# Kernel optimization log

Hardware: AMD Instinct MI355X
Metric: run time of the kernel (lower is better)

Reference implementation:

```python
import jax, jax.numpy as jnp
import numpy as np

B, T = 8, 1024
D = 256          # n_embd
NH = 4           # n_head
MULT = 4         # mlp_internal_dim_multiplier
GRID = 32        # grid_size, T == GRID*GRID
NLAYER = 3
N = D * MULT // NH   # sparse head dim = 256
EPS = 1e-5


def _freqs_2d(h, w, dim, theta=10000.0):
    # matches get_freqs_2d_fixed: returns (h*w, dim//2) complex64
    dim_half = dim // 2
    freqs = 1.0 / theta ** (np.arange(0, dim_half, 2, dtype=np.float32) / dim_half)
    fx = np.outer(np.arange(w, dtype=np.float32), freqs)
    fy = np.outer(np.arange(h, dtype=np.float32), freqs)
    cx = np.exp(1j * fx).astype(np.complex64)          # (w, dim_half/2)
    cy = np.exp(1j * fy).astype(np.complex64)          # (h, dim_half/2)
    gx = np.broadcast_to(cx[None, :, :], (h, w, cx.shape[-1]))
    gy = np.broadcast_to(cy[:, None, :], (h, w, cy.shape[-1]))
    return np.concatenate([gx, gy], axis=-1).reshape(h * w, -1)

FREQS = jnp.asarray(_freqs_2d(GRID, GRID, N))  # (T, N//2) complex64


def _rope(x):
    # x: (B, nh, T, N) real -> complex pairs, rotate, back to real
    xc = x.reshape(*x.shape[:-1], -1, 2)
    xc = jax.lax.complex(xc[..., 0], xc[..., 1])       # (B, nh, T, N/2)
    xr = xc * FREQS[None, None, :, :]
    out = jnp.stack([jnp.real(xr), jnp.imag(xr)], axis=-1)
    return out.reshape(x.shape).astype(x.dtype)


def _ln(x):
    # LayerNorm over last dim, no affine (biased variance, like torch)
    m = jnp.mean(x, axis=-1, keepdims=True)
    v = jnp.var(x, axis=-1, keepdims=True)
    return (x - m) / jnp.sqrt(v + EPS)


def setup_inputs() -> dict:
    key = jax.random.key(0)
    ks = jax.random.split(key, 6)
    std = 0.02
    return {
        "inputs": jax.random.normal(ks[0], (B, T), dtype=jnp.float32),
        "in_w": jax.random.normal(ks[1], (D, 1), dtype=jnp.float32) * std,
        "in_b": jnp.zeros((D,), dtype=jnp.float32),
        "encoder": jax.random.normal(ks[2], (NH, D, N), dtype=jnp.float32) * std,
        "encoder_v": jax.random.normal(ks[3], (NH, D, N), dtype=jnp.float32) * std,
        "decoder": jax.random.normal(ks[4], (NH * N, D), dtype=jnp.float32) * std,
        "out_w": jax.random.normal(ks[5], (1, D), dtype=jnp.float32) * std,
        "out_b": jnp.zeros((1,), dtype=jnp.float32),
    }


def reference(inputs, in_w, in_b, encoder, encoder_v, decoder, out_w, out_b):
    # input projection: (B,T,1) @ (1,D) + b -> (B,T,D)
    x = inputs[..., None] * in_w[None, None, :, 0].swapaxes(-1, -1)  # placeholder
    x = inputs[..., None] @ in_w.T + in_b                            # (B,T,D)
    x = _ln(x)
    scale = 1.0 / jnp.sqrt(jnp.asarray(N, dtype=x.dtype))
    for _ in range(NLAYER):
        # encoder: (B,T,D) x (nh,D,N) -> (B,nh,T,N)
        x_sparse = jax.nn.relu(jnp.einsum('btd,hdn->bhtn', x, encoder))
        QR = _rope(x_sparse)
        KR = _rope(x_sparse)
        scores = jnp.einsum('bhtn,bhsn->bhts', QR, KR) * scale       # (B,nh,T,T)
        attn = jax.nn.softmax(scores, axis=-1)
        yKV = jnp.einsum('bhts,bsd->bhtd', attn, x)                  # V = x, broadcast over heads
        yKV = _ln(yKV)
        y_sparse = jax.nn.relu(jnp.einsum('bhtd,hdn->bhtn', yKV, encoder_v))
        xy_sparse = x_sparse * y_sparse                              # (B,nh,T,N)
        # (B,nh,T,N) -> (B,T,nh*N) @ (nh*N,D) -> (B,T,D)
        yMLP = xy_sparse.transpose(0, 2, 1, 3).reshape(B, T, NH * N) @ decoder
        x = _ln(x + _ln(yMLP))
    logits = x @ out_w.T + out_b                                     # (B,T,1)
    return logits
```

## Files before the change

### kernel.cpp

```cpp
#include <hip/hip_runtime.h>
#include <hip/hip_bf16.h>
#include <math.h>

#define B_ 8
#define T_ 1024
#define D_ 256
#define NH_ 4
#define N_ 256
#define EPS_ 1e-5f

typedef __attribute__((ext_vector_type(8))) short short8_t;
typedef __attribute__((ext_vector_type(4))) float floatx4;

__device__ inline unsigned short f2bf(float f) {
    unsigned u = __builtin_bit_cast(unsigned, f);
    u += 0x7FFFu + ((u >> 16) & 1u);
    return (unsigned short)(u >> 16);
}
__device__ inline float bf2f(unsigned short h) {
    return __builtin_bit_cast(float, (unsigned)h << 16);
}

__device__ inline void gload_lds16(const unsigned short* g, unsigned short* l) {
    __builtin_amdgcn_global_load_lds(
        (const __attribute__((address_space(1))) unsigned int*)g,
        (__attribute__((address_space(3))) unsigned int*)l, 16, 0, 0);
}

__device__ inline float2 block_stats_256(float v, float* red) {
    float s1 = v, s2 = v * v;
    #pragma unroll
    for (int o = 32; o > 0; o >>= 1) { s1 += __shfl_down(s1, o); s2 += __shfl_down(s2, o); }
    int wave = threadIdx.x >> 6, lane = threadIdx.x & 63;
    __syncthreads();
    if (lane == 0) { red[wave] = s1; red[4 + wave] = s2; }
    __syncthreads();
    float S1 = red[0] + red[1] + red[2] + red[3];
    float S2 = red[4] + red[5] + red[6] + red[7];
    float mean = S1 * (1.f / 256.f);
    float var  = S2 * (1.f / 256.f) - mean * mean;
    return make_float2(mean, var);
}

__global__ __launch_bounds__(256) void k_wT(
    const float* __restrict__ in, unsigned short* __restrict__ outh,
    unsigned short* __restrict__ outl, int R, int C)
{
    __shared__ float tile[64][65];
    int c0 = blockIdx.x * 64, r0 = blockIdx.y * 64, h = blockIdx.z;
    in += (size_t)h * R * C;
    for (int i = threadIdx.x; i < 4096; i += 256) {
        int r = i >> 6, c = i & 63;
        tile[r][c] = in[(size_t)(r0 + r) * C + c0 + c];
    }
    __syncthreads();
    for (int i = threadIdx.x; i < 4096; i += 256) {
        int c = i >> 6, r = i & 63;
        float v = tile[r][c];
        unsigned short hb = f2bf(v);
        size_t o = (size_t)(h * C + c0 + c) * R + r0 + r;
        outh[o] = hb;
        outl[o] = f2bf(v - bf2f(hb));
    }
}

__global__ __launch_bounds__(256) void k_input_ln(
    const float* __restrict__ inputs, const float* __restrict__ in_w,
    const float* __restrict__ in_b, float* __restrict__ x,
    unsigned short* __restrict__ xh, unsigned short* __restrict__ xl)
{
    __shared__ float red[8];
    int row = blockIdx.x;
    int d = threadIdx.x;
    float v = inputs[row] * in_w[d] + in_b[d];
    float2 mv = block_stats_256(v, red);
    float o = (v - mv.x) * rsqrtf(mv.y + EPS_);
    size_t idx = (size_t)row * D_ + d;
    x[idx] = o;
    unsigned short hb = f2bf(o);
    xh[idx] = hb;
    xl[idx] = f2bf(o - bf2f(hb));
}

#define PG 40
template<int MODE>
__global__ __launch_bounds__(256, 2) void k_gemm_mfma(
    const unsigned short* __restrict__ Ah, const unsigned short* __restrict__ Al,
    const unsigned short* __restrict__ Wh, const unsigned short* __restrict__ Wl,
    const unsigned short* __restrict__ xsh, const unsigned short* __restrict__ xsl,
    unsigned short* __restrict__ outh, unsigned short* __restrict__ outl,
    float* __restrict__ outf,
    unsigned short* __restrict__ qrh, unsigned short* __restrict__ qrl)
{
    constexpr int K = (MODE == 2) ? 1024 : 256;
    __shared__ unsigned short As_h[128 * PG], As_l[128 * PG];
    __shared__ unsigned short Ws_h[128 * PG], Ws_l[128 * PG];
    int tid = threadIdx.x;
    int w = tid >> 6, lane = tid & 63, quad = lane >> 4, l16 = lane & 15;
    int wm = w >> 1, wn = w & 1;
    int m0 = blockIdx.y * 128, n0x = blockIdx.x * 128;
    size_t a_row0, w_row0, out_row0;
    int col0;
    int koff = 0, kend = K;
    if (MODE == 1) {
        int bh = blockIdx.z;
        a_row0 = (size_t)bh * 1024 + m0;
        w_row0 = (size_t)((bh & 3) * 256 + n0x);
        out_row0 = (size_t)(bh >> 2) * 1024 + m0;
        col0 = (bh & 3) * 256 + n0x;
    } else {
        a_row0 = m0; w_row0 = n0x; out_row0 = m0; col0 = n0x;
        if (MODE == 2) { koff = blockIdx.z * 256; kend = koff + 256; }
    }
    floatx4 acc[4][4];
    #pragma unroll
    for (int mt = 0; mt < 4; mt++)
        #pragma unroll
        for (int nt = 0; nt < 4; nt++)
            acc[mt][nt] = (floatx4){0.f, 0.f, 0.f, 0.f};

    for (int k0 = koff; k0 < kend; k0 += 32) {
        #pragma unroll
        for (int it = 0; it < 2; it++) {
            int fl = tid + it * 256;
            int row = fl >> 2, ch = fl & 3;
            size_t ga = (a_row0 + row) * (size_t)K + k0 + ch * 8;
            size_t gw = (w_row0 + row) * (size_t)K + k0 + ch * 8;
            *(short8_t*)&As_h[row * PG + ch * 8] = *(const short8_t*)(Ah + ga);
            *(short8_t*)&As_l[row * PG + ch * 8] = *(const short8_t*)(Al + ga);
            *(short8_t*)&Ws_h[row * PG + ch * 8] = *(const short8_t*)(Wh + gw);
            *(short8_t*)&Ws_l[row * PG + ch * 8] = *(const short8_t*)(Wl + gw);
        }
        __syncthreads();
        short8_t afh[4], afl[4], bfh[4], bfl[4];
        #pragma unroll
        for (int mt = 0; mt < 4; mt++) {
            afh[mt] = *(const short8_t*)&As_h[(wm * 64 + mt * 16 + l16) * PG + quad * 8];
            afl[mt] = *(const short8_t*)&As_l[(wm * 64 + mt * 16 + l16) * PG + quad * 8];
        }
        #pragma unroll
        for (int nt = 0; nt < 4; nt++) {
            bfh[nt] = *(const short8_t*)&Ws_h[(wn * 64 + nt * 16 + l16) * PG + quad * 8];
            bfl[nt] = *(const short8_t*)&Ws_l[(wn * 64 + nt * 16 + l16) * PG + quad * 8];
        }
        #pragma unroll
        for (int mt = 0; mt < 4; mt++)
            #pragma unroll
            for (int nt = 0; nt < 4; nt++) {
                acc[mt][nt] = __builtin_amdgcn_mfma_f32_16x16x32_bf16(afh[mt], bfh[nt], acc[mt][nt], 0, 0, 0);
                acc[mt][nt] = __builtin_amdgcn_mfma_f32_16x16x32_bf16(afh[mt], bfl[nt], acc[mt][nt], 0, 0, 0);
                acc[mt][nt] = __builtin_amdgcn_mfma_f32_16x16x32_bf16(afl[mt], bfh[nt], acc[mt][nt], 0, 0, 0);
            }
        __syncthreads();
    }

    #pragma unroll
    for (int mt = 0; mt < 4; mt++) {
        #pragma unroll
        for (int r = 0; r < 4; r++) {
            size_t grow = out_row0 + wm * 64 + mt * 16 + quad * 4 + r;
            #pragma unroll
            for (int nt = 0; nt < 4; nt++) {
                int gcol = col0 + wn * 64 + nt * 16 + l16;
                float v = acc[mt][nt][r];
                if (MODE == 0) {
                    v = fmaxf(v, 0.f);
                    size_t o = grow * 1024 + gcol;
                    unsigned short hb = f2bf(v);
                    outh[o] = hb;
                    outl[o] = f2bf(v - bf2f(hb));
                    float vp = __shfl_xor(v, 1);
                    int n = gcol & 255, h = gcol >> 8;
                    int t = (int)(grow & 1023), b = (int)(grow >> 10);
                    int p = n >> 1, j = p & 63;
                    int pos = (p < 64) ? (t & 31) : (t >> 5);
                    float f = __expf((float)j * -0.14391156f);
                    float ang = (float)pos * f;
                    float sn = __sinf(ang), cs = __cosf(ang);
                    float ro = (n & 1) ? (vp * sn + v * cs) : (v * cs - vp * sn);
                    size_t qo = (((size_t)b * NH_ + h) * T_ + t) * N_ + n;
                    unsigned short qb = f2bf(ro);
                    qrh[qo] = qb;
                    qrl[qo] = f2bf(ro - bf2f(qb));
                } else if (MODE == 1) {
                    float y = fmaxf(v, 0.f);
                    size_t o = grow * 1024 + gcol;
                    float xv = bf2f(xsh[o]) + bf2f(xsl[o]);
                    float p = xv * y;
                    unsigned short hb = f2bf(p);
                    outh[o] = hb;
                    outl[o] = f2bf(p - bf2f(hb));
                } else {
                    outf[(size_t)blockIdx.z * 2097152 + grow * 256 + gcol] = v;
                }
            }
        }
    }
}

__global__ __launch_bounds__(256) void k_xT(const float* __restrict__ x,
                                            unsigned short* __restrict__ Vfh,
                                            unsigned short* __restrict__ Vfl)
{
    __shared__ float tile[64][65];
    int t0 = blockIdx.x * 64, d0 = blockIdx.y * 64, b = blockIdx.z;
    const float* src = x + ((size_t)b * T_ + t0) * D_ + d0;
    for (int i = threadIdx.x; i < 1024; i += 256) {
        int r = i >> 4, c = i & 15;
        float4 v = *(const float4*)(src + (size_t)r * D_ + c * 4);
        tile[r][c * 4 + 0] = v.x;
        tile[r][c * 4 + 1] = v.y;
        tile[r][c * 4 + 2] = v.z;
        tile[r][c * 4 + 3] = v.w;
    }
    __syncthreads();
    for (int i = threadIdx.x; i < 1024; i += 256) {
        int d = i >> 4, c = i & 15;
        int tg = t0 + c * 4;
        int jj = tg >> 5, qd = (tg >> 3) & 3, i8 = tg & 7;
        int dg = d0 + d;
        int tn = dg >> 4, s16 = dg & 15;
        size_t o = (((size_t)b * 32 + jj) * 16 + tn) * 512 + (qd * 16 + s16) * 8 + i8;
        float v0 = tile[c * 4 + 0][d], v1 = tile[c * 4 + 1][d];
        float v2 = tile[c * 4 + 2][d], v3 = tile[c * 4 + 3][d];
        ushort4 oh, ol;
        oh.x = f2bf(v0); ol.x = f2bf(v0 - bf2f(oh.x));
        oh.y = f2bf(v1); ol.y = f2bf(v1 - bf2f(oh.y));
        oh.z = f2bf(v2); ol.z = f2bf(v2 - bf2f(oh.z));
        oh.w = f2bf(v3); ol.w = f2bf(v3 - bf2f(oh.w));
        *(ushort4*)(Vfh + o) = oh;
        *(ushort4*)(Vfl + o) = ol;
    }
}

#define PPW 36

__global__ __launch_bounds__(512, 1) void k_attn_mfma(
    const unsigned short* __restrict__ qr_h, const unsigned short* __restrict__ qr_l,
    const unsigned short* __restrict__ Vf_h, const unsigned short* __restrict__ Vf_l,
    unsigned short* __restrict__ ykvh, unsigned short* __restrict__ ykvl)
{
    __shared__ unsigned short K_h[2][16 * 512];
    __shared__ unsigned short K_l[2][16 * 512];
    __shared__ unsigned short V_h[2][16 * 512];
    __shared__ unsigned short V_l[2][16 * 512];
    __shared__ unsigned short P_h[8][16 * PPW];
    __shared__ unsigned short P_l[8][16 * PPW];

    int tid = threadIdx.x;
    int w = tid >> 6, lane = tid & 63, quad = lane >> 4, l16 = lane & 15;
    int gid = blockIdx.x;
    int bh = gid & 31, tile = gid >> 5, b = bh >> 2;
    int t0q = tile * 128;
    const unsigned short* qhb = qr_h + (size_t)bh * T_ * N_;
    const unsigned short* qlb = qr_l + (size_t)bh * T_ * N_;
    const unsigned short* vhb = Vf_h + (size_t)b * 32 * 16 * 512;
    const unsigned short* vlb = Vf_l + (size_t)b * 32 * 16 * 512;

    short8_t qfh[8], qfl[8];
    #pragma unroll
    for (int kc = 0; kc < 8; kc++) {
        size_t o = (size_t)(t0q + w * 16 + l16) * N_ + kc * 32 + quad * 8;
        qfh[kc] = *(const short8_t*)(qhb + o);
        qfl[kc] = *(const short8_t*)(qlb + o);
    }

    floatx4 O[16];
    #pragma unroll
    for (int tn = 0; tn < 16; tn++) O[tn] = (floatx4){0.f, 0.f, 0.f, 0.f};
    float lst[4] = {0.f, 0.f, 0.f, 0.f};
    const float scale = 0.0625f;

    #pragma unroll
    for (int s = 0; s < 2; s++) {
        int slot = w * 2 + s;
        int ct = slot >> 3, kc = slot & 7;
        size_t go = (size_t)(ct * 16 + l16) * N_ + kc * 32 + quad * 8;
        gload_lds16(qhb + go, &K_h[0][slot * 512]);
        gload_lds16(qlb + go, &K_l[0][slot * 512]);
        size_t vo = ((size_t)slot << 9) + lane * 8;
        gload_lds16(vhb + vo, &V_h[0][slot * 512]);
        gload_lds16(vlb + vo, &V_l[0][slot * 512]);
    }

    for (int j = 0; j < 32; j++) {
        int buf = j & 1;
        __syncthreads();
        if (j < 31) {
            #pragma unroll
            for (int s = 0; s < 2; s++) {
                int slot = w * 2 + s;
                int ct = slot >> 3, kc = slot & 7;
                size_t go = (size_t)((j + 1) * 32 + ct * 16 + l16) * N_ + kc * 32 + quad * 8;
                gload_lds16(qhb + go, &K_h[buf ^ 1][slot * 512]);
                gload_lds16(qlb + go, &K_l[buf ^ 1][slot * 512]);
                size_t vo = ((size_t)((j + 1) * 16 + slot) << 9) + lane * 8;
                gload_lds16(vhb + vo, &V_h[buf ^ 1][slot * 512]);
                gload_lds16(vlb + vo, &V_l[buf ^ 1][slot * 512]);
            }
        }

        floatx4 sc[2];
        #pragma unroll
        for (int ct = 0; ct < 2; ct++) {
            floatx4 a_hh = (floatx4){0.f, 0.f, 0.f, 0.f};
            floatx4 a_hl = (floatx4){0.f, 0.f, 0.f, 0.f};
            floatx4 a_lh = (floatx4){0.f, 0.f, 0.f, 0.f};
            #pragma unroll
            for (int kc = 0; kc < 8; kc++) {
                short8_t bkh = *(const short8_t*)&K_h[buf][(ct * 8 + kc) * 512 + lane * 8];
                short8_t bkl = *(const short8_t*)&K_l[buf][(ct * 8 + kc) * 512 + lane * 8];
                a_hh = __builtin_amdgcn_mfma_f32_16x16x32_bf16(qfh[kc], bkh, a_hh, 0, 0, 0);
                a_hl = __builtin_amdgcn_mfma_f32_16x16x32_bf16(qfh[kc], bkl, a_hl, 0, 0, 0);
                a_lh = __builtin_amdgcn_mfma_f32_16x16x32_bf16(qfl[kc], bkh, a_lh, 0, 0, 0);
            }
            sc[ct] = (a_hh + a_hl) + a_lh;
        }

        #pragma unroll
        for (int r = 0; r < 4; r++) {
            float p0 = __expf(sc[0][r] * scale - 8.f);
            float p1 = __expf(sc[1][r] * scale - 8.f);
            lst[r] += p0 + p1;
            unsigned short p0h = f2bf(p0), p1h = f2bf(p1);
            P_h[w][(quad * 4 + r) * PPW + l16]      = p0h;
            P_h[w][(quad * 4 + r) * PPW + 16 + l16] = p1h;
            P_l[w][(quad * 4 + r) * PPW + l16]      = f2bf(p0 - bf2f(p0h));
            P_l[w][(quad * 4 + r) * PPW + 16 + l16] = f2bf(p1 - bf2f(p1h));
        }

        short8_t pah = *(const short8_t*)&P_h[w][l16 * PPW + quad * 8];
        short8_t pal = *(const short8_t*)&P_l[w][l16 * PPW + quad * 8];

        #pragma unroll
        for (int tn = 0; tn < 16; tn++) {
            short8_t vbh = *(const short8_t*)&V_h[buf][tn * 512 + lane * 8];
            short8_t vbl = *(const short8_t*)&V_l[buf][tn * 512 + lane * 8];
            O[tn] = __builtin_amdgcn_mfma_f32_16x16x32_bf16(pah, vbh, O[tn], 0, 0, 0);
            O[tn] = __builtin_amdgcn_mfma_f32_16x16x32_bf16(pah, vbl, O[tn], 0, 0, 0);
            O[tn] = __builtin_amdgcn_mfma_f32_16x16x32_bf16(pal, vbh, O[tn], 0, 0, 0);
        }
    }

    size_t obase = ((size_t)bh * T_ + t0q + w * 16) * D_;
    #pragma unroll
    for (int r = 0; r < 4; r++) {
        float lsum = lst[r];
        #pragma unroll
        for (int o = 1; o < 16; o <<= 1) lsum += __shfl_xor(lsum, o);
        float li = 1.f / lsum;
        float s1 = 0.f, s2 = 0.f;
        #pragma unroll
        for (int tn = 0; tn < 16; tn++) { float v = O[tn][r]; s1 += v; s2 += v * v; }
        #pragma unroll
        for (int o = 1; o < 16; o <<= 1) { s1 += __shfl_xor(s1, o); s2 += __shfl_xor(s2, o); }
        float mean = s1 * li * (1.f / 256.f);
        float e2   = s2 * li * li * (1.f / 256.f);
        float var  = e2 - mean * mean;
        float rs = rsqrtf(var + EPS_);
        float a = li * rs, bb = mean * rs;
        int row = quad * 4 + r;
        #pragma unroll
        for (int tn = 0; tn < 16; tn++) {
            float v = O[tn][r] * a - bb;
            size_t o = obase + (size_t)row * D_ + tn * 16 + l16;
            unsigned short hb = f2bf(v);
            ykvh[o] = hb;
            ykvl[o] = f2bf(v - bf2f(hb));
        }
    }
}

__global__ __launch_bounds__(256) void k_resid_ln(float* __restrict__ x,
                                                  const float* __restrict__ ymlp,
                                                  unsigned short* __restrict__ xh,
                                                  unsigned short* __restrict__ xl)
{
    __shared__ float red[8];
    int row = blockIdx.x, d = threadIdx.x;
    size_t o = (size_t)row * D_ + d;
    float y = ymlp[o] + ymlp[o + 2097152] + ymlp[o + 2 * 2097152] + ymlp[o + 3 * 2097152];
    float2 mv1 = block_stats_256(y, red);
    float v = x[o] + (y - mv1.x) * rsqrtf(mv1.y + EPS_);
    float2 mv2 = block_stats_256(v, red);
    float out = (v - mv2.x) * rsqrtf(mv2.y + EPS_);
    x[o] = out;
    unsigned short hb = f2bf(out);
    xh[o] = hb;
    xl[o] = f2bf(out - bf2f(hb));
}

__global__ __launch_bounds__(256) void k_logits(
    const float* __restrict__ x, const float* __restrict__ out_w,
    const float* __restrict__ out_b, float* __restrict__ out)
{
    __shared__ float red[4];
    int row = blockIdx.x, d = threadIdx.x;
    float v = x[(size_t)row * D_ + d] * out_w[d];
    #pragma unroll
    for (int o = 32; o > 0; o >>= 1) v += __shfl_down(v, o);
    int wave = d >> 6, lane = d & 63;
    if (lane == 0) red[wave] = v;
    __syncthreads();
    if (d == 0) out[row] = red[0] + red[1] + red[2] + red[3] + out_b[0];
}

extern "C" void kernel_launch(void* const* d_in, const int* in_sizes, int n_in,
                              void* d_out, int out_size, void* d_ws, size_t ws_size,
                              hipStream_t stream)
{
    (void)in_sizes; (void)n_in; (void)out_size;
    if (ws_size < ((size_t)115 << 20)) return;

    const float* inputs    = (const float*)d_in[0];
    const float* in_w      = (const float*)d_in[1];
    const float* in_b      = (const float*)d_in[2];
    const float* encoder   = (const float*)d_in[3];
    const float* encoder_v = (const float*)d_in[4];
    const float* decoder   = (const float*)d_in[5];
    const float* out_w     = (const float*)d_in[6];
    const float* out_b     = (const float*)d_in[7];

    char* wsb = (char*)d_ws;
    float* x             = (float*)(wsb);
    unsigned short* x_h  = (unsigned short*)(wsb + ((size_t)8  << 20));
    unsigned short* x_l  = (unsigned short*)(wsb + ((size_t)12 << 20));
    unsigned short* Vf_h = x_h;
    unsigned short* Vf_l = x_l;
    unsigned short* xs_h = (unsigned short*)(wsb + ((size_t)16 << 20));
    unsigned short* xs_l = (unsigned short*)(wsb + ((size_t)32 << 20));
    float* ymlp          = (float*)(wsb + ((size_t)16 << 20));
    unsigned short* qr_h = (unsigned short*)(wsb + ((size_t)48 << 20));
    unsigned short* qr_l = (unsigned short*)(wsb + ((size_t)64 << 20));
    unsigned short* xy_h = qr_h;
    unsigned short* xy_l = qr_l;
    unsigned short* ykv_h = (unsigned short*)(wsb + ((size_t)80 << 20));
    unsigned short* ykv_l = (unsigned short*)(wsb + ((size_t)96 << 20));
    char* wbase = wsb + ((size_t)112 << 20);
    unsigned short* encT_h = (unsigned short*)(wbase);
    unsigned short* encT_l = (unsigned short*)(wbase + 0x80000);
    unsigned short* evT_h  = (unsigned short*)(wbase + 2 * 0x80000);
    unsigned short* evT_l  = (unsigned short*)(wbase + 3 * 0x80000);
    unsigned short* decT_h = (unsigned short*)(wbase + 4 * 0x80000);
    unsigned short* decT_l = (unsigned short*)(wbase + 5 * 0x80000);

    k_wT<<<dim3(4, 4, 4), 256, 0, stream>>>(encoder,   encT_h, encT_l, 256, 256);
    k_wT<<<dim3(4, 4, 4), 256, 0, stream>>>(encoder_v, evT_h,  evT_l,  256, 256);
    k_wT<<<dim3(4, 16, 1), 256, 0, stream>>>(decoder,  decT_h, decT_l, 1024, 256);

    k_input_ln<<<B_ * T_, 256, 0, stream>>>(inputs, in_w, in_b, x, x_h, x_l);
    for (int l = 0; l < 3; l++) {
        k_gemm_mfma<0><<<dim3(8, 64, 1), 256, 0, stream>>>(
            x_h, x_l, encT_h, encT_l, nullptr, nullptr, xs_h, xs_l, nullptr, qr_h, qr_l);
        k_xT<<<dim3(16, 4, 8), 256, 0, stream>>>(x, Vf_h, Vf_l);
        k_attn_mfma<<<256, 512, 0, stream>>>(qr_h, qr_l, Vf_h, Vf_l, ykv_h, ykv_l);
        k_gemm_mfma<1><<<dim3(2, 8, 32), 256, 0, stream>>>(
            ykv_h, ykv_l, evT_h, evT_l, xs_h, xs_l, xy_h, xy_l, nullptr, nullptr, nullptr);
        k_gemm_mfma<2><<<dim3(2, 64, 4), 256, 0, stream>>>(
            xy_h, xy_l, decT_h, decT_l, nullptr, nullptr, nullptr, nullptr, ymlp, nullptr, nullptr);
        k_resid_ln<<<B_ * T_, 256, 0, stream>>>(x, ymlp, x_h, x_l);
    }
    k_logits<<<B_ * T_, 256, 0, stream>>>(x, out_w, out_b, (float*)d_out);
}
```

Baseline: 727.3 us.

## Shrink attention blocks to 256 threads, single-buffer K/V, add MFMA priority hints

Attention blocks now hold 64 queries with 4 waves instead of 128 with 8, giving 512 blocks and allowing two blocks per CU. K/V staging drops from double to single buffering, with a barrier before and after each load. s_setprio is raised around the MFMA sections. Co-resident blocks are meant to hide load latency in place of explicit prefetch, but each block now loads K/V for half as many queries, so global and LDS traffic per query doubles and loads no longer overlap compute within a block.

```diff
diff --git a/kernel.cpp b/kernel.cpp
--- a/kernel.cpp
+++ b/kernel.cpp
@@ -235,23 +235,23 @@
 
 #define PPW 36
 
-__global__ __launch_bounds__(512, 1) void k_attn_mfma(
+__global__ __launch_bounds__(256, 2) void k_attn_mfma(
     const unsigned short* __restrict__ qr_h, const unsigned short* __restrict__ qr_l,
     const unsigned short* __restrict__ Vf_h, const unsigned short* __restrict__ Vf_l,
     unsigned short* __restrict__ ykvh, unsigned short* __restrict__ ykvl)
 {
-    __shared__ unsigned short K_h[2][16 * 512];
-    __shared__ unsigned short K_l[2][16 * 512];
-    __shared__ unsigned short V_h[2][16 * 512];
-    __shared__ unsigned short V_l[2][16 * 512];
-    __shared__ unsigned short P_h[8][16 * PPW];
-    __shared__ unsigned short P_l[8][16 * PPW];
+    __shared__ unsigned short K_h[16 * 512];
+    __shared__ unsigned short K_l[16 * 512];
+    __shared__ unsigned short V_h[16 * 512];
+    __shared__ unsigned short V_l[16 * 512];
+    __shared__ unsigned short P_h[4][16 * PPW];
+    __shared__ unsigned short P_l[4][16 * PPW];
 
     int tid = threadIdx.x;
     int w = tid >> 6, lane = tid & 63, quad = lane >> 4, l16 = lane & 15;
     int gid = blockIdx.x;
     int bh = gid & 31, tile = gid >> 5, b = bh >> 2;
-    int t0q = tile * 128;
+    int t0q = tile * 64;
     const unsigned short* qhb = qr_h + (size_t)bh * T_ * N_;
     const unsigned short* qlb = qr_l + (size_t)bh * T_ * N_;
     const unsigned short* vhb = Vf_h + (size_t)b * 32 * 16 * 512;
@@ -271,36 +271,23 @@
     float lst[4] = {0.f, 0.f, 0.f, 0.f};
     const float scale = 0.0625f;
 
-    #pragma unroll
-    for (int s = 0; s < 2; s++) {
-        int slot = w * 2 + s;
-        int ct = slot >> 3, kc = slot & 7;
-        size_t go = (size_t)(ct * 16 + l16) * N_ + kc * 32 + quad * 8;
-        gload_lds16(qhb + go, &K_h[0][slot * 512]);
-        gload_lds16(qlb + go, &K_l[0][slot * 512]);
-        size_t vo = ((size_t)slot << 9) + lane * 8;
-        gload_lds16(vhb + vo, &V_h[0][slot * 512]);
-        gload_lds16(vlb + vo, &V_l[0][slot * 512]);
-    }
-
     for (int j = 0; j < 32; j++) {
-        int buf = j & 1;
         __syncthreads();
-        if (j < 31) {
-            #pragma unroll
-            for (int s = 0; s < 2; s++) {
-                int slot = w * 2 + s;
-                int ct = slot >> 3, kc = slot & 7;
-                size_t go = (size_t)((j + 1) * 32 + ct * 16 + l16) * N_ + kc * 32 + quad * 8;
-                gload_lds16(qhb + go, &K_h[buf ^ 1][slot * 512]);
-                gload_lds16(qlb + go, &K_l[buf ^ 1][slot * 512]);
-                size_t vo = ((size_t)((j + 1) * 16 + slot) << 9) + lane * 8;
-                gload_lds16(vhb + vo, &V_h[buf ^ 1][slot * 512]);
-                gload_lds16(vlb + vo, &V_l[buf ^ 1][slot * 512]);
-            }
-        }
+        #pragma unroll
+        for (int s = 0; s < 4; s++) {
+            int slot = w * 4 + s;
+            int ct = slot >> 3, kc = slot & 7;
+            size_t go = (size_t)(j * 32 + ct * 16 + l16) * N_ + kc * 32 + quad * 8;
+            gload_lds16(qhb + go, &K_h[slot * 512]);
+            gload_lds16(qlb + go, &K_l[slot * 512]);
+            size_t vo = ((size_t)(j * 16 + slot) << 9) + lane * 8;
+            gload_lds16(vhb + vo, &V_h[slot * 512]);
+            gload_lds16(vlb + vo, &V_l[slot * 512]);
+        }
+        __syncthreads();
 
         floatx4 sc[2];
+        __builtin_amdgcn_s_setprio(1);
         #pragma unroll
         for (int ct = 0; ct < 2; ct++) {
             floatx4 a_hh = (floatx4){0.f, 0.f, 0.f, 0.f};
@@ -308,14 +295,15 @@
             floatx4 a_lh = (floatx4){0.f, 0.f, 0.f, 0.f};
             #pragma unroll
             for (int kc = 0; kc < 8; kc++) {
-                short8_t bkh = *(const short8_t*)&K_h[buf][(ct * 8 + kc) * 512 + lane * 8];
-                short8_t bkl = *(const short8_t*)&K_l[buf][(ct * 8 + kc) * 512 + lane * 8];
+                short8_t bkh = *(const short8_t*)&K_h[(ct * 8 + kc) * 512 + lane * 8];
+                short8_t bkl = *(const short8_t*)&K_l[(ct * 8 + kc) * 512 + lane * 8];
                 a_hh = __builtin_amdgcn_mfma_f32_16x16x32_bf16(qfh[kc], bkh, a_hh, 0, 0, 0);
                 a_hl = __builtin_amdgcn_mfma_f32_16x16x32_bf16(qfh[kc], bkl, a_hl, 0, 0, 0);
                 a_lh = __builtin_amdgcn_mfma_f32_16x16x32_bf16(qfl[kc], bkh, a_lh, 0, 0, 0);
             }
             sc[ct] = (a_hh + a_hl) + a_lh;
         }
+        __builtin_amdgcn_s_setprio(0);
 
         #pragma unroll
         for (int r = 0; r < 4; r++) {
@@ -332,14 +320,16 @@
         short8_t pah = *(const short8_t*)&P_h[w][l16 * PPW + quad * 8];
         short8_t pal = *(const short8_t*)&P_l[w][l16 * PPW + quad * 8];
 
+        __builtin_amdgcn_s_setprio(1);
         #pragma unroll
         for (int tn = 0; tn < 16; tn++) {
-            short8_t vbh = *(const short8_t*)&V_h[buf][tn * 512 + lane * 8];
-            short8_t vbl = *(const short8_t*)&V_l[buf][tn * 512 + lane * 8];
+            short8_t vbh = *(const short8_t*)&V_h[tn * 512 + lane * 8];
+            short8_t vbl = *(const short8_t*)&V_l[tn * 512 + lane * 8];
             O[tn] = __builtin_amdgcn_mfma_f32_16x16x32_bf16(pah, vbh, O[tn], 0, 0, 0);
             O[tn] = __builtin_amdgcn_mfma_f32_16x16x32_bf16(pah, vbl, O[tn], 0, 0, 0);
             O[tn] = __builtin_amdgcn_mfma_f32_16x16x32_bf16(pal, vbh, O[tn], 0, 0, 0);
         }
+        __builtin_amdgcn_s_setprio(0);
     }
 
     size_t obase = ((size_t)bh * T_ + t0q + w * 16) * D_;
@@ -453,7 +443,7 @@
         k_gemm_mfma<0><<<dim3(8, 64, 1), 256, 0, stream>>>(
             x_h, x_l, encT_h, encT_l, nullptr, nullptr, xs_h, xs_l, nullptr, qr_h, qr_l);
         k_xT<<<dim3(16, 4, 8), 256, 0, stream>>>(x, Vf_h, Vf_l);
-        k_attn_mfma<<<256, 512, 0, stream>>>(qr_h, qr_l, Vf_h, Vf_l, ykv_h, ykv_l);
+        k_attn_mfma<<<512, 256, 0, stream>>>(qr_h, qr_l, Vf_h, Vf_l, ykv_h, ykv_l);
         k_gemm_mfma<1><<<dim3(2, 8, 32), 256, 0, stream>>>(
             ykv_h, ykv_l, evT_h, evT_l, xs_h, xs_l, xy_h, xy_l, nullptr, nullptr, nullptr);
         k_gemm_mfma<2><<<dim3(2, 64, 4), 256, 0, stream>>>(
```

Result: no change. 725.1 us (-0.3%).

## Give each attention wave two query row tiles to reuse K/V fragments

Applied to the files above, without the earlier changes.

The attention kernel now runs with 4 waves per block instead of 8, and each wave handles two 16-row query tiles. Every K and V fragment read from LDS is therefore used for twice as many MFMAs, which halves LDS read traffic per FLOP. Each wave also issues more cooperative loads per stage. s_setprio is raised around the MFMA sections to favour matrix issue. In exchange, register pressure roughly doubles (two O accumulator sets and two Q fragment sets), and each block has fewer waves to hide latency.

```diff
diff --git a/kernel.cpp b/kernel.cpp
--- a/kernel.cpp
+++ b/kernel.cpp
@@ -235,7 +235,7 @@
 
 #define PPW 36
 
-__global__ __launch_bounds__(512, 1) void k_attn_mfma(
+__global__ __launch_bounds__(256, 1) void k_attn_mfma(
     const unsigned short* __restrict__ qr_h, const unsigned short* __restrict__ qr_l,
     const unsigned short* __restrict__ Vf_h, const unsigned short* __restrict__ Vf_l,
     unsigned short* __restrict__ ykvh, unsigned short* __restrict__ ykvl)
@@ -244,8 +244,8 @@
     __shared__ unsigned short K_l[2][16 * 512];
     __shared__ unsigned short V_h[2][16 * 512];
     __shared__ unsigned short V_l[2][16 * 512];
-    __shared__ unsigned short P_h[8][16 * PPW];
-    __shared__ unsigned short P_l[8][16 * PPW];
+    __shared__ unsigned short P_h[4][16 * PPW];
+    __shared__ unsigned short P_l[4][16 * PPW];
 
     int tid = threadIdx.x;
     int w = tid >> 6, lane = tid & 63, quad = lane >> 4, l16 = lane & 15;
@@ -257,23 +257,27 @@
     const unsigned short* vhb = Vf_h + (size_t)b * 32 * 16 * 512;
     const unsigned short* vlb = Vf_l + (size_t)b * 32 * 16 * 512;
 
-    short8_t qfh[8], qfl[8];
-    #pragma unroll
-    for (int kc = 0; kc < 8; kc++) {
-        size_t o = (size_t)(t0q + w * 16 + l16) * N_ + kc * 32 + quad * 8;
-        qfh[kc] = *(const short8_t*)(qhb + o);
-        qfl[kc] = *(const short8_t*)(qlb + o);
-    }
-
-    floatx4 O[16];
-    #pragma unroll
-    for (int tn = 0; tn < 16; tn++) O[tn] = (floatx4){0.f, 0.f, 0.f, 0.f};
-    float lst[4] = {0.f, 0.f, 0.f, 0.f};
+    short8_t qfh[2][8], qfl[2][8];
+    #pragma unroll
+    for (int mt = 0; mt < 2; mt++)
+        #pragma unroll
+        for (int kc = 0; kc < 8; kc++) {
+            size_t o = (size_t)(t0q + w * 32 + mt * 16 + l16) * N_ + kc * 32 + quad * 8;
+            qfh[mt][kc] = *(const short8_t*)(qhb + o);
+            qfl[mt][kc] = *(const short8_t*)(qlb + o);
+        }
+
+    floatx4 O[2][16];
+    #pragma unroll
+    for (int mt = 0; mt < 2; mt++)
+        #pragma unroll
+        for (int tn = 0; tn < 16; tn++) O[mt][tn] = (floatx4){0.f, 0.f, 0.f, 0.f};
+    float lst[2][4] = {{0.f, 0.f, 0.f, 0.f}, {0.f, 0.f, 0.f, 0.f}};
     const float scale = 0.0625f;
 
     #pragma unroll
-    for (int s = 0; s < 2; s++) {
-        int slot = w * 2 + s;
+    for (int s = 0; s < 4; s++) {
+        int slot = w * 4 + s;
         int ct = slot >> 3, kc = slot & 7;
         size_t go = (size_t)(ct * 16 + l16) * N_ + kc * 32 + quad * 8;
         gload_lds16(qhb + go, &K_h[0][slot * 512]);
@@ -288,8 +292,8 @@
         __syncthreads();
         if (j < 31) {
             #pragma unroll
-            for (int s = 0; s < 2; s++) {
-                int slot = w * 2 + s;
+            for (int s = 0; s < 4; s++) {
+                int slot = w * 4 + s;
                 int ct = slot >> 3, kc = slot & 7;
                 size_t go = (size_t)((j + 1) * 32 + ct * 16 + l16) * N_ + kc * 32 + quad * 8;
                 gload_lds16(qhb + go, &K_h[buf ^ 1][slot * 512]);
@@ -300,73 +304,93 @@
             }
         }
 
-        floatx4 sc[2];
+        floatx4 sc[2][2];
+        __builtin_amdgcn_s_setprio(1);
         #pragma unroll
         for (int ct = 0; ct < 2; ct++) {
-            floatx4 a_hh = (floatx4){0.f, 0.f, 0.f, 0.f};
-            floatx4 a_hl = (floatx4){0.f, 0.f, 0.f, 0.f};
-            floatx4 a_lh = (floatx4){0.f, 0.f, 0.f, 0.f};
+            floatx4 a_hh0 = (floatx4){0.f, 0.f, 0.f, 0.f};
+            floatx4 a_hl0 = (floatx4){0.f, 0.f, 0.f, 0.f};
+            floatx4 a_lh0 = (floatx4){0.f, 0.f, 0.f, 0.f};
+            floatx4 a_hh1 = (floatx4){0.f, 0.f, 0.f, 0.f};
+            floatx4 a_hl1 = (floatx4){0.f, 0.f, 0.f, 0.f};
+            floatx4 a_lh1 = (floatx4){0.f, 0.f, 0.f, 0.f};
             #pragma unroll
             for (int kc = 0; kc < 8; kc++) {
                 short8_t bkh = *(const short8_t*)&K_h[buf][(ct * 8 + kc) * 512 + lane * 8];
                 short8_t bkl = *(const short8_t*)&K_l[buf][(ct * 8 + kc) * 512 + lane * 8];
-                a_hh = __builtin_amdgcn_mfma_f32_16x16x32_bf16(qfh[kc], bkh, a_hh, 0, 0, 0);
-                a_hl = __builtin_amdgcn_mfma_f32_16x16x32_bf16(qfh[kc], bkl, a_hl, 0, 0, 0);
-                a_lh = __builtin_amdgcn_mfma_f32_16x16x32_bf16(qfl[kc], bkh, a_lh, 0, 0, 0);
-            }
-            sc[ct] = (a_hh + a_hl) + a_lh;
-        }
-
-        #pragma unroll
-        for (int r = 0; r < 4; r++) {
-            float p0 = __expf(sc[0][r] * scale - 8.f);
-            float p1 = __expf(sc[1][r] * scale - 8.f);
-            lst[r] += p0 + p1;
-            unsigned short p0h = f2bf(p0), p1h = f2bf(p1);
-            P_h[w][(quad * 4 + r) * PPW + l16]      = p0h;
-            P_h[w][(quad * 4 + r) * PPW + 16 + l16] = p1h;
-            P_l[w][(quad * 4 + r) * PPW + l16]      = f2bf(p0 - bf2f(p0h));
-            P_l[w][(quad * 4 + r) * PPW + 16 + l16] = f2bf(p1 - bf2f(p1h));
-        }
-
-        short8_t pah = *(const short8_t*)&P_h[w][l16 * PPW + quad * 8];
-        short8_t pal = *(const short8_t*)&P_l[w][l16 * PPW + quad * 8];
-
+                a_hh0 = __builtin_amdgcn_mfma_f32_16x16x32_bf16(qfh[0][kc], bkh, a_hh0, 0, 0, 0);
+                a_hh1 = __builtin_amdgcn_mfma_f32_16x16x32_bf16(qfh[1][kc], bkh, a_hh1, 0, 0, 0);
+                a_hl0 = __builtin_amdgcn_mfma_f32_16x16x32_bf16(qfh[0][kc], bkl, a_hl0, 0, 0, 0);
+                a_hl1 = __builtin_amdgcn_mfma_f32_16x16x32_bf16(qfh[1][kc], bkl, a_hl1, 0, 0, 0);
+                a_lh0 = __builtin_amdgcn_mfma_f32_16x16x32_bf16(qfl[0][kc], bkh, a_lh0, 0, 0, 0);
+                a_lh1 = __builtin_amdgcn_mfma_f32_16x16x32_bf16(qfl[1][kc], bkh, a_lh1, 0, 0, 0);
+            }
+            sc[0][ct] = (a_hh0 + a_hl0) + a_lh0;
+            sc[1][ct] = (a_hh1 + a_hl1) + a_lh1;
+        }
+        __builtin_amdgcn_s_setprio(0);
+
+        short8_t pah[2], pal[2];
+        #pragma unroll
+        for (int mt = 0; mt < 2; mt++) {
+            #pragma unroll
+            for (int r = 0; r < 4; r++) {
+                float p0 = __expf(sc[mt][0][r] * scale - 8.f);
+                float p1 = __expf(sc[mt][1][r] * scale - 8.f);
+                lst[mt][r] += p0 + p1;
+                unsigned short p0h = f2bf(p0), p1h = f2bf(p1);
+                P_h[w][(quad * 4 + r) * PPW + l16]      = p0h;
+                P_h[w][(quad * 4 + r) * PPW + 16 + l16] = p1h;
+                P_l[w][(quad * 4 + r) * PPW + l16]      = f2bf(p0 - bf2f(p0h));
+                P_l[w][(quad * 4 + r) * PPW + 16 + l16] = f2bf(p1 - bf2f(p1h));
+            }
+            pah[mt] = *(const short8_t*)&P_h[w][l16 * PPW + quad * 8];
+            pal[mt] = *(const short8_t*)&P_l[w][l16 * PPW + quad * 8];
+        }
+
+        __builtin_amdgcn_s_setprio(1);
         #pragma unroll
         for (int tn = 0; tn < 16; tn++) {
             short8_t vbh = *(const short8_t*)&V_h[buf][tn * 512 + lane * 8];
             short8_t vbl = *(const short8_t*)&V_l[buf][tn * 512 + lane * 8];
-            O[tn] = __builtin_amdgcn_mfma_f32_16x16x32_bf16(pah, vbh, O[tn], 0, 0, 0);
-            O[tn] = __builtin_amdgcn_mfma_f32_16x16x32_bf16(pah, vbl, O[tn], 0, 0, 0);
-            O[tn] = __builtin_amdgcn_mfma_f32_16x16x32_bf16(pal, vbh, O[tn], 0, 0, 0);
-        }
-    }
-
-    size_t obase = ((size_t)bh * T_ + t0q + w * 16) * D_;
-    #pragma unroll
-    for (int r = 0; r < 4; r++) {
-        float lsum = lst[r];
-        #pragma unroll
-        for (int o = 1; o < 16; o <<= 1) lsum += __shfl_xor(lsum, o);
-        float li = 1.f / lsum;
-        float s1 = 0.f, s2 = 0.f;
-        #pragma unroll
-        for (int tn = 0; tn < 16; tn++) { float v = O[tn][r]; s1 += v; s2 += v * v; }
-        #pragma unroll
-        for (int o = 1; o < 16; o <<= 1) { s1 += __shfl_xor(s1, o); s2 += __shfl_xor(s2, o); }
-        float mean = s1 * li * (1.f / 256.f);
-        float e2   = s2 * li * li * (1.f / 256.f);
-        float var  = e2 - mean * mean;
-        float rs = rsqrtf(var + EPS_);
-        float a = li * rs, bb = mean * rs;
-        int row = quad * 4 + r;
-        #pragma unroll
-        for (int tn = 0; tn < 16; tn++) {
-            float v = O[tn][r] * a - bb;
-            size_t o = obase + (size_t)row * D_ + tn * 16 + l16;
-            unsigned short hb = f2bf(v);
-            ykvh[o] = hb;
-            ykvl[o] = f2bf(v - bf2f(hb));
+            O[0][tn] = __builtin_amdgcn_mfma_f32_16x16x32_bf16(pah[0], vbh, O[0][tn], 0, 0, 0);
+            O[1][tn] = __builtin_amdgcn_mfma_f32_16x16x32_bf16(pah[1], vbh, O[1][tn], 0, 0, 0);
+            O[0][tn] = __builtin_amdgcn_mfma_f32_16x16x32_bf16(pah[0], vbl, O[0][tn], 0, 0, 0);
+            O[1][tn] = __builtin_amdgcn_mfma_f32_16x16x32_bf16(pah[1], vbl, O[1][tn], 0, 0, 0);
+            O[0][tn] = __builtin_amdgcn_mfma_f32_16x16x32_bf16(pal[0], vbh, O[0][tn], 0, 0, 0);
+            O[1][tn] = __builtin_amdgcn_mfma_f32_16x16x32_bf16(pal[1], vbh, O[1][tn], 0, 0, 0);
+        }
+        __builtin_amdgcn_s_setprio(0);
+    }
+
+    #pragma unroll
+    for (int mt = 0; mt < 2; mt++) {
+        size_t obase = ((size_t)bh * T_ + t0q + w * 32 + mt * 16) * D_;
+        #pragma unroll
+        for (int r = 0; r < 4; r++) {
+            float lsum = lst[mt][r];
+            #pragma unroll
+            for (int o = 1; o < 16; o <<= 1) lsum += __shfl_xor(lsum, o);
+            float li = 1.f / lsum;
+            float s1 = 0.f, s2 = 0.f;
+            #pragma unroll
+            for (int tn = 0; tn < 16; tn++) { float v = O[mt][tn][r]; s1 += v; s2 += v * v; }
+            #pragma unroll
+            for (int o = 1; o < 16; o <<= 1) { s1 += __shfl_xor(s1, o); s2 += __shfl_xor(s2, o); }
+            float mean = s1 * li * (1.f / 256.f);
+            float e2   = s2 * li * li * (1.f / 256.f);
+            float var  = e2 - mean * mean;
+            float rs = rsqrtf(var + EPS_);
+            float a = li * rs, bb = mean * rs;
+            int row = quad * 4 + r;
+            #pragma unroll
+            for (int tn = 0; tn < 16; tn++) {
+                float v = O[mt][tn][r] * a - bb;
+                size_t o = obase + (size_t)row * D_ + tn * 16 + l16;
+                unsigned short hb = f2bf(v);
+                ykvh[o] = hb;
+                ykvl[o] = f2bf(v - bf2f(hb));
+            }
         }
     }
 }
@@ -453,7 +477,7 @@
         k_gemm_mfma<0><<<dim3(8, 64, 1), 256, 0, stream>>>(
             x_h, x_l, encT_h, encT_l, nullptr, nullptr, xs_h, xs_l, nullptr, qr_h, qr_l);
         k_xT<<<dim3(16, 4, 8), 256, 0, stream>>>(x, Vf_h, Vf_l);
-        k_attn_mfma<<<256, 512, 0, stream>>>(qr_h, qr_l, Vf_h, Vf_l, ykv_h, ykv_l);
+        k_attn_mfma<<<256, 256, 0, stream>>>(qr_h, qr_l, Vf_h, Vf_l, ykv_h, ykv_l);
         k_gemm_mfma<1><<<dim3(2, 8, 32), 256, 0, stream>>>(
             ykv_h, ykv_l, evT_h, evT_l, xs_h, xs_l, xy_h, xy_l, nullptr, nullptr, nullptr);
         k_gemm_mfma<2><<<dim3(2, 64, 4), 256, 0, stream>>>(
```

Result: slower. 827.8 us (+13.8%).
